# Kernel tuning notes

Hardware: AMD Instinct MI355X
Metric: run time of the kernel (lower is better)

## Reference

```python
import math
import jax, jax.numpy as jnp
import numpy as np

FACTOR = math.pi ** (-0.5)
C1 = math.sqrt(3.0 / 8.0) * FACTOR
C2 = math.sqrt(3.0 / 4.0) * FACTOR
EPS = 1e-9


def _cg_111():
    # Clebsch-Gordan <1 m1 ; 1 m2 | 1 m3>, indexed [m1+1, m2+1, m3+1]
    s = 1.0 / math.sqrt(2.0)
    cg = np.zeros((3, 3, 3), np.float32)
    cg[2, 1, 2] = s   # <1,1;1,0|1,1>
    cg[1, 2, 2] = -s  # <1,0;1,1|1,1>
    cg[2, 0, 1] = s   # <1,1;1,-1|1,0>
    cg[0, 2, 1] = -s  # <1,-1;1,1|1,0>
    cg[1, 0, 0] = s   # <1,0;1,-1|1,-1>
    cg[0, 1, 0] = -s  # <1,-1;1,0|1,-1>
    return jnp.asarray(cg)


def spherical_l1(r):
    # r: [n,p,q,3] -> Y1, Y2: [n,p,q,3] (real/imag parts of Y_1^m)
    rx, ry, rz = r[..., 0], r[..., 1], r[..., 2]
    Y1 = jnp.stack([C1 * rx, C2 * rz, -C1 * rx], axis=-1)
    Y2 = jnp.stack([-C1 * ry, jnp.zeros_like(ry), -C1 * ry], axis=-1)
    zero = (jnp.linalg.norm(r, axis=-1) == 0.0)[..., None]
    Y1 = jnp.where(zero, 1.0, Y1)
    Y2 = jnp.where(zero, 1.0, Y2)
    return Y1, Y2


def setup_inputs() -> dict:
    key = jax.random.key(0)
    ks = jax.random.split(key, 12)
    n, p, fr, fin, fout = 16, 256, 64, 64, 64
    rbf = jax.random.normal(ks[0], (n, p, p, fr), jnp.float32)
    uv = jax.random.normal(ks[1], (n, p, p, 3), jnp.float32)
    uv = uv / (jnp.linalg.norm(uv, axis=-1, keepdims=True) + 1e-12)
    inp1 = jax.random.normal(ks[2], (n, p, 3, fin), jnp.float32)
    inp2 = jax.random.normal(ks[3], (n, p, 3, fin), jnp.float32)
    mask = jnp.ones((n, p), jnp.bool_)
    sc = 0.08
    W1 = jax.random.normal(ks[4], (fin, fr), jnp.float32) * sc
    b1 = jax.random.normal(ks[5], (fin,), jnp.float32) * sc
    W2 = jax.random.normal(ks[6], (fin, fin), jnp.float32) * sc
    b2 = jax.random.normal(ks[7], (fin,), jnp.float32) * sc
    W_si = jax.random.normal(ks[8], (fout, fin), jnp.float32) * sc
    bias_b = jax.random.normal(ks[9], (1,), jnp.float32) * sc
    return {"rbf": rbf, "unit_vector": uv, "inp1": inp1, "inp2": inp2,
            "mask": mask, "coef": _cg_111(), "W1": W1, "b1": b1,
            "W2": W2, "b2": b2, "W_si": W_si, "bias_b": bias_b}


def reference(rbf, unit_vector, inp1, inp2, mask, coef, W1, b1, W2, b2, W_si, bias_b):
    m = mask[:, :, None, None]  # broadcast over q and last dims
    Y1, Y2 = spherical_l1(unit_vector)
    Y1 = jnp.where(m, Y1, 0.0)
    Y2 = jnp.where(m, Y2, 0.0)
    # radial embedding MLP: Linear -> ReLU -> Linear
    radial = jnp.einsum('npqr,fr->npqf', rbf, W1) + b1
    radial = jax.nn.relu(radial)
    radial = jnp.einsum('npqf,gf->npqg', radial, W2) + b2
    radial = jnp.where(m, radial, 0.0)

    def tp(Y, inp):
        return jnp.einsum('abc,npqb,npqf,npaf->nqcf', coef, Y, radial, inp,
                          optimize='optimal')

    out1 = tp(Y1, inp1) - tp(Y2, inp2)
    out2 = tp(Y2, inp1) + tp(Y1, inp2)
    # norm over {stack, c} dims, keepdim on c -> [n,q,1,f]
    norm = jnp.sqrt(jnp.sum(out1 ** 2 + out2 ** 2, axis=-2, keepdims=True))
    out1 = out1 / (norm + EPS)
    out2 = out2 / (norm + EPS)
    # gated self-interaction
    out1 = jnp.einsum('nqcf,gf->nqcg', out1, W_si)
    out2 = jnp.einsum('nqcf,gf->nqcg', out2, W_si)
    norm2 = jnp.sqrt(jnp.sum(out1 ** 2 + out2 ** 2, axis=-2))  # [n,q,g]
    nonlinear = jax.nn.relu(norm2 + bias_b[0])[:, :, None, :]  # [n,q,1,g]
    return out1 * nonlinear, out2 * nonlinear
```

## Files before the change

### kernel.cpp

```cpp
#include <hip/hip_runtime.h>
#include <hip/hip_bf16.h>

typedef __attribute__((ext_vector_type(8))) short short8;
typedef __attribute__((ext_vector_type(4))) float f32x4;
typedef __attribute__((ext_vector_type(4))) unsigned int u32x4;

#define MFMA16(A, B, C) __builtin_amdgcn_mfma_f32_16x16x32_bf16(A, B, C, 0, 0, 0)

__device__ __forceinline__ unsigned int pkbf(float lo, float hi) {
  unsigned int ul = (unsigned int)__bfloat16_as_ushort(__float2bfloat16(lo));
  unsigned int uh = (unsigned int)__bfloat16_as_ushort(__float2bfloat16(hi));
  return ul | (uh << 16);
}

union S8U { short8 s; u32x4 u; };
__device__ __forceinline__ short8 mk8(unsigned int a, unsigned int b,
                                      unsigned int c, unsigned int d) {
  S8U t; u32x4 v = {a, b, c, d}; t.u = v; return t.s;
}

constexpr float SU = 0.24430125595146f;
constexpr float SW = 0.34549414947134f;


__global__ __launch_bounds__(256) void tfield_partial(
    const float* __restrict__ rbf,  const float* __restrict__ uv,
    const float* __restrict__ inp1, const float* __restrict__ inp2,
    const float* __restrict__ W1,   const float* __restrict__ b1,
    const float* __restrict__ W2,   const float* __restrict__ b2,
    float* __restrict__ ws)
{
  __shared__ __align__(16) unsigned char pool[27008];
  unsigned int* wfrag = (unsigned int*)pool;
  unsigned int* hbuf  = (unsigned int*)(pool + 12288);
  float* ibuf  = (float*)(pool + 20480);
  float* biasL = (float*)(pool + 26624);
  float* accL  = (float*)pool;

  const int tid = threadIdx.x;
  const int l   = tid & 63;
  const int w   = tid >> 6;
  const int g   = l >> 4;
  const int qh  = l & 15;

  const int bid = blockIdx.x;
  const int wid = ((((bid & 7) << 5) | (bid >> 5)) << 2) | ((bid >> 3) & 3);
  const int nq  = wid >> 2;
  const int fh  = (wid >> 1) & 1;
  const int ph  = wid & 1;
  const int n   = nq >> 4;
  const int q0  = (nq & 15) << 4;

  #pragma unroll
  for (int k = 0; k < 3; ++k) {
    const int slot = tid + (k << 8);
    const int fi = slot >> 6;
    const int ll = slot & 63;
    const int gg = ll >> 4;
    const int qq = ll & 15;
    const float* src;
    if (fi < 8) {
      src = W1 + ((fi >> 1) * 16 + qq) * 64 + (fi & 1) * 32 + gg * 8;
    } else {
      const int fj = fi - 8;
      src = W2 + (((fh << 1) + (fj >> 1)) * 16 + qq) * 64 + (fj & 1) * 32 + gg * 8;
    }
    f32x4 x0 = *(const f32x4*)src;
    f32x4 x1 = *(const f32x4*)(src + 4);
    u32x4 vv = {pkbf(x0[0], x0[1]), pkbf(x0[2], x0[3]), pkbf(x1[0], x1[1]), pkbf(x1[2], x1[3])};
    *(u32x4*)(wfrag + ((fi << 6) + ll) * 4) = vv;
  }
  if (tid < 96) biasL[tid] = (tid < 64) ? b1[tid] : b2[(fh << 5) + tid - 64];
  __syncthreads();

  const float* bL1 = biasL;
  const float* bL2 = biasL + 64;

  f32x4 accT[2][6];
  #pragma unroll
  for (int a = 0; a < 2; ++a)
    #pragma unroll
    for (int j = 0; j < 6; ++j) accT[a][j] = (f32x4){0.f, 0.f, 0.f, 0.f};

  const size_t nbase = (size_t)n * 256;
  const int pbase = (ph << 7) + w;

  const int sl = (l < 24) ? l : l - 24;
  const float* isrcb = (l < 24) ? inp1 : inp2;
  const int ioff = (sl >> 3) * 64 + (fh << 5) + ((sl & 7) << 2);

  unsigned int* hrow = hbuf + (w << 9) + (qh << 5);
  float* iw = ibuf + w * 384;
  const int swz = qh & 7;

  f32x4 rn0, rn1, rn2, rn3;
  { const float* rr = rbf + ((nbase + pbase) * 256 + q0 + qh) * 64 + (g << 3);
    rn0 = *(const f32x4*)rr;        rn1 = *(const f32x4*)(rr + 4);
    rn2 = *(const f32x4*)(rr + 32); rn3 = *(const f32x4*)(rr + 36); }
  f32x4 stage_v = {0.f, 0.f, 0.f, 0.f};
  if (l < 48) stage_v = *(const f32x4*)(isrcb + (nbase + pbase) * 192 + ioff);
  float uc0, uc1, uc2, un0, un1, un2;
  { const float* u = uv + ((nbase + pbase) * 256 + q0 + qh) * 3;
    uc0 = u[0]; uc1 = u[1]; uc2 = u[2]; }

  short8 rf0 = mk8(pkbf(rn0[0], rn0[1]), pkbf(rn0[2], rn0[3]), pkbf(rn1[0], rn1[1]), pkbf(rn1[2], rn1[3]));
  short8 rf1 = mk8(pkbf(rn2[0], rn2[1]), pkbf(rn2[2], rn2[3]), pkbf(rn3[0], rn3[1]), pkbf(rn3[2], rn3[3]));
  f32x4 h4[4];
  #pragma unroll
  for (int mt = 0; mt < 4; ++mt) {
    f32x4 c = *(const f32x4*)(bL1 + (mt << 4) + (g << 2));
    short8 a0 = *(const short8*)(wfrag + (((mt << 1) + 0) * 64 + l) * 4);
    short8 a1 = *(const short8*)(wfrag + (((mt << 1) + 1) * 64 + l) * 4);
    c = MFMA16(a0, rf0, c);
    c = MFMA16(a1, rf1, c);
    h4[mt] = c;
  }
  if (l < 48) *(f32x4*)(iw + (l << 2)) = stage_v;
  #pragma unroll
  for (int mt = 0; mt < 4; ++mt) {
    const float e0 = fmaxf(h4[mt][0], 0.f);
    const float e1 = fmaxf(h4[mt][1], 0.f);
    const float e2 = fmaxf(h4[mt][2], 0.f);
    const float e3 = fmaxf(h4[mt][3], 0.f);
    const int base = ((((mt << 1) + (g >> 1)) ^ swz) << 2) + ((g & 1) << 1);
    hrow[base]     = pkbf(e0, e1);
    hrow[base + 1] = pkbf(e2, e3);
  }
  short8 hb0 = *(const short8*)(hrow + (((0 + g) ^ swz) << 2));
  short8 hb1 = *(const short8*)(hrow + (((4 + g) ^ swz) << 2));
  { const float* rr = rbf + ((nbase + pbase + 4) * 256 + q0 + qh) * 64 + (g << 3);
    rn0 = *(const f32x4*)rr;        rn1 = *(const f32x4*)(rr + 4);
    rn2 = *(const f32x4*)(rr + 32); rn3 = *(const f32x4*)(rr + 36); }
  if (l < 48) stage_v = *(const f32x4*)(isrcb + (nbase + pbase + 4) * 192 + ioff);
  { const float* u = uv + ((nbase + pbase + 4) * 256 + q0 + qh) * 3;
    un0 = u[0]; un1 = u[1]; un2 = u[2]; }

  for (int s = 0; s < 32; ++s) {
    const int s2 = (s + 2 < 32) ? s + 2 : 31;

    rf0 = mk8(pkbf(rn0[0], rn0[1]), pkbf(rn0[2], rn0[3]), pkbf(rn1[0], rn1[1]), pkbf(rn1[2], rn1[3]));
    rf1 = mk8(pkbf(rn2[0], rn2[1]), pkbf(rn2[2], rn2[3]), pkbf(rn3[0], rn3[1]), pkbf(rn3[2], rn3[3]));
    #pragma unroll
    for (int mt = 0; mt < 4; ++mt) {
      f32x4 c = *(const f32x4*)(bL1 + (mt << 4) + (g << 2));
      short8 a0 = *(const short8*)(wfrag + (((mt << 1) + 0) * 64 + l) * 4);
      short8 a1 = *(const short8*)(wfrag + (((mt << 1) + 1) * 64 + l) * 4);
      c = MFMA16(a0, rf0, c);
      c = MFMA16(a1, rf1, c);
      h4[mt] = c;
    }
    { const float* rr = rbf + ((nbase + pbase + (s2 << 2)) * 256 + q0 + qh) * 64 + (g << 3);
      rn0 = *(const f32x4*)rr;        rn1 = *(const f32x4*)(rr + 4);
      rn2 = *(const f32x4*)(rr + 32); rn3 = *(const f32x4*)(rr + 36); }

    f32x4 cc0, cc1;
    {
      f32x4 c = *(const f32x4*)(bL2 + (g << 2));
      short8 wa0 = *(const short8*)(wfrag + ((8 + 0) * 64 + l) * 4);
      short8 wa1 = *(const short8*)(wfrag + ((8 + 1) * 64 + l) * 4);
      c = MFMA16(wa0, hb0, c);
      c = MFMA16(wa1, hb1, c);
      cc0 = c;
      c = *(const f32x4*)(bL2 + 16 + (g << 2));
      wa0 = *(const short8*)(wfrag + ((8 + 2) * 64 + l) * 4);
      wa1 = *(const short8*)(wfrag + ((8 + 3) * 64 + l) * 4);
      c = MFMA16(wa0, hb0, c);
      c = MFMA16(wa1, hb1, c);
      cc1 = c;
    }

    const float su  = SU * uc0;
    const float sv  = SU * uc1;
    const float swc = SW * uc2;
    uc0 = un0; uc1 = un1; uc2 = un2;
    { const float* u = uv + ((nbase + pbase + (s2 << 2)) * 256 + q0 + qh) * 3;
      un0 = u[0]; un1 = u[1]; un2 = u[2]; }

    const float* ib = iw + ((s & 1) * 192) + (g << 2);
    #pragma unroll
    for (int mt2l = 0; mt2l < 2; ++mt2l) {
      const f32x4 A0 = *(const f32x4*)(ib + (mt2l << 4));
      const f32x4 A1 = *(const f32x4*)(ib + (mt2l << 4) + 32);
      const f32x4 A2 = *(const f32x4*)(ib + (mt2l << 4) + 64);
      const f32x4 B0 = *(const f32x4*)(ib + (mt2l << 4) + 96);
      const f32x4 B1 = *(const f32x4*)(ib + (mt2l << 4) + 128);
      const f32x4 B2 = *(const f32x4*)(ib + (mt2l << 4) + 160);
      const f32x4 cc = mt2l ? cc1 : cc0;

      const f32x4 t1 = su * A1, t2 = sv * B1;
      const f32x4 t3 = su * B1, t4 = sv * A1;
      const f32x4 g10 = (t1 + t2) - swc * A0;
      const f32x4 g11 = su * (A0 + A2) - sv * (B0 - B2);
      const f32x4 g12 = (t1 - t2) + swc * A2;
      const f32x4 g20 = (t3 - t4) - swc * B0;
      const f32x4 g21 = sv * (A0 - A2) + su * (B0 + B2);
      const f32x4 g22 = (t3 + t4) + swc * B2;
      accT[mt2l][0] += cc * g10;
      accT[mt2l][1] += cc * g11;
      accT[mt2l][2] += cc * g12;
      accT[mt2l][3] += cc * g20;
      accT[mt2l][4] += cc * g21;
      accT[mt2l][5] += cc * g22;
    }

    if (l < 48) *(f32x4*)(iw + (((s + 1) & 1) * 192) + (l << 2)) = stage_v;
    if (l < 48) stage_v = *(const f32x4*)(isrcb + (nbase + pbase + (s2 << 2)) * 192 + ioff);

    #pragma unroll
    for (int mt = 0; mt < 4; ++mt) {
      const float e0 = fmaxf(h4[mt][0], 0.f);
      const float e1 = fmaxf(h4[mt][1], 0.f);
      const float e2 = fmaxf(h4[mt][2], 0.f);
      const float e3 = fmaxf(h4[mt][3], 0.f);
      const int base = ((((mt << 1) + (g >> 1)) ^ swz) << 2) + ((g & 1) << 1);
      hrow[base]     = pkbf(e0, e1);
      hrow[base + 1] = pkbf(e2, e3);
    }
    hb0 = *(const short8*)(hrow + (((0 + g) ^ swz) << 2));
    hb1 = *(const short8*)(hrow + (((4 + g) ^ swz) << 2));
  }

  __syncthreads();
  for (int i = tid; i < 3072; i += 256) accL[i] = 0.f;
  __syncthreads();
  for (int t = 0; t < 4; ++t) {
    if (w == t) {
      #pragma unroll
      for (int mt2l = 0; mt2l < 2; ++mt2l)
        #pragma unroll
        for (int v = 0; v < 4; ++v) {
          float* dst = accL + (((qh << 5) + (mt2l << 4) + (g << 2) + v) * 6);
          #pragma unroll
          for (int j = 0; j < 6; ++j) dst[j] += accT[mt2l][j][v];
        }
    }
    __syncthreads();
  }
  float* wp = ws + (size_t)wid * 3072;
  for (int i = tid; i < 3072; i += 256) wp[i] = accL[i];
}

__global__ __launch_bounds__(512) void tfield_finish(
    const float* __restrict__ ws, const float* __restrict__ Wsi,
    const float* __restrict__ biasb, float* __restrict__ out)
{
  __shared__ __align__(16) float accL[6144];
  __shared__ __align__(16) float wsiT[4096];

  const int tid = threadIdx.x;
  const int l   = tid & 63;
  const int w   = tid >> 6;
  const int nq  = blockIdx.x;
  const int n   = nq >> 4;
  const int q0  = (nq & 15) << 4;

  const float* c00 = ws + (size_t)(nq * 4 + 0) * 3072;
  const float* c01 = c00 + 3072;
  const float* c10 = c00 + 6144;
  const float* c11 = c00 + 9216;
  for (int i = tid; i < 3072; i += 512) {
    const int qhh = i / 192;
    const int rem = i - qhh * 192;
    accL[qhh * 384 + rem]       = c00[i] + c01[i];
    accL[qhh * 384 + 192 + rem] = c10[i] + c11[i];
  }
  #pragma unroll
  for (int k = 0; k < 8; ++k) {
    const int f = (w << 3) + k;
    wsiT[(f << 6) + l] = Wsi[(l << 6) + f];
  }
  __syncthreads();

  #pragma unroll
  for (int rep = 0; rep < 2; ++rep) {
    const int qq = w + (rep << 3);
    float* xp = accL + ((qq << 6) + l) * 6;
    const float x0 = xp[0], x1 = xp[1], x2 = xp[2], x3 = xp[3], x4 = xp[4], x5 = xp[5];
    const float nrm = sqrtf(x0*x0 + x1*x1 + x2*x2 + x3*x3 + x4*x4 + x5*x5);
    const float sc = 1.f / (nrm + 1e-9f);
    xp[0] = x0 * sc; xp[1] = x1 * sc; xp[2] = x2 * sc;
    xp[3] = x3 * sc; xp[4] = x4 * sc; xp[5] = x5 * sc;
  }
  __syncthreads();

  const float bb = biasb[0];
  #pragma unroll
  for (int rep = 0; rep < 2; ++rep) {
    const int qq = w + (rep << 3);
    const float* arow = accL + (qq << 6) * 6;
    float pj0 = 0, pj1 = 0, pj2 = 0, pj3 = 0, pj4 = 0, pj5 = 0;
    for (int f = 0; f < 64; ++f) {
      const float wv = wsiT[(f << 6) + l];
      const float* ap = arow + f * 6;
      pj0 += ap[0] * wv; pj1 += ap[1] * wv; pj2 += ap[2] * wv;
      pj3 += ap[3] * wv; pj4 += ap[4] * wv; pj5 += ap[5] * wv;
    }
    const float s2 = pj0*pj0 + pj1*pj1 + pj2*pj2 + pj3*pj3 + pj4*pj4 + pj5*pj5;
    const float nl = fmaxf(sqrtf(s2) + bb, 0.f);
    const int q = q0 + qq;
    float* o1 = out + (size_t)((n * 256 + q) * 3) * 64 + l;
    float* o2 = o1 + 786432;
    o1[0]   = pj0 * nl;
    o1[64]  = pj1 * nl;
    o1[128] = pj2 * nl;
    o2[0]   = pj3 * nl;
    o2[64]  = pj4 * nl;
    o2[128] = pj5 * nl;
  }
}

__global__ __launch_bounds__(512) void tfield_kernel(
    const float* __restrict__ rbf,  const float* __restrict__ uv,
    const float* __restrict__ inp1, const float* __restrict__ inp2,
    const float* __restrict__ W1,   const float* __restrict__ b1,
    const float* __restrict__ W2,   const float* __restrict__ b2,
    const float* __restrict__ Wsi,  const float* __restrict__ biasb,
    float* __restrict__ out)
{
  __shared__ __align__(16) unsigned char pool[40960];
  unsigned int* wfrag = (unsigned int*)pool;
  unsigned int* hbuf  = (unsigned int*)(pool + 16384);
  float* accL = (float*)pool;
  float* wsiT = (float*)(pool + 24576);

  const int tid = threadIdx.x;
  const int l   = tid & 63;
  const int w   = tid >> 6;
  const int g   = l >> 4;
  const int qh  = l & 15;
  const int n   = blockIdx.x >> 4;
  const int q0  = (blockIdx.x & 15) << 4;

  {
    const int row = ((w >> 1) << 4) + qh;
    const int kb  = ((w & 1) << 5) + (g << 3);
    const float* s1 = W1 + row * 64 + kb;
    f32x4 x0 = *(const f32x4*)s1;
    f32x4 x1 = *(const f32x4*)(s1 + 4);
    u32x4 v1 = {pkbf(x0[0], x0[1]), pkbf(x0[2], x0[3]), pkbf(x1[0], x1[1]), pkbf(x1[2], x1[3])};
    *(u32x4*)(wfrag + ((w << 6) + l) * 4) = v1;
    const float* s2 = W2 + row * 64 + kb;
    x0 = *(const f32x4*)s2;
    x1 = *(const f32x4*)(s2 + 4);
    u32x4 v2 = {pkbf(x0[0], x0[1]), pkbf(x0[2], x0[3]), pkbf(x1[0], x1[1]), pkbf(x1[2], x1[3])};
    *(u32x4*)(wfrag + (((8 + w) << 6) + l) * 4) = v2;
  }
  __syncthreads();

  float accT[4][4][6];
  #pragma unroll
  for (int a = 0; a < 4; ++a)
    #pragma unroll
    for (int b = 0; b < 4; ++b)
      #pragma unroll
      for (int j = 0; j < 6; ++j) accT[a][b][j] = 0.f;

  const size_t nbase = (size_t)n * 256;
  const float* rr0 = rbf + ((nbase + w) * 256 + q0 + qh) * 64 + (g << 3);
  f32x4 nx0 = *(const f32x4*)(rr0);
  f32x4 nx1 = *(const f32x4*)(rr0 + 4);
  f32x4 nx2 = *(const f32x4*)(rr0 + 32);
  f32x4 nx3 = *(const f32x4*)(rr0 + 36);

  unsigned int* hrow = hbuf + ((w << 4) + qh) * 32;
  const int swz = qh & 7;

  for (int s = 0; s < 32; ++s) {
    const int p = (s << 3) + w;
    f32x4 r0 = nx0, r1 = nx1, r2 = nx2, r3 = nx3;
    {
      const int pn = (s < 31) ? p + 8 : p;
      const float* rr = rbf + ((nbase + pn) * 256 + q0 + qh) * 64 + (g << 3);
      nx0 = *(const f32x4*)(rr);
      nx1 = *(const f32x4*)(rr + 4);
      nx2 = *(const f32x4*)(rr + 32);
      nx3 = *(const f32x4*)(rr + 36);
    }
    const float* uvp = uv + ((nbase + p) * 256 + q0 + qh) * 3;
    const float su = SU * uvp[0];
    const float sv = SU * uvp[1];
    const float swc = SW * uvp[2];

    const short8 rf0 = mk8(pkbf(r0[0], r0[1]), pkbf(r0[2], r0[3]), pkbf(r1[0], r1[1]), pkbf(r1[2], r1[3]));
    const short8 rf1 = mk8(pkbf(r2[0], r2[1]), pkbf(r2[2], r2[3]), pkbf(r3[0], r3[1]), pkbf(r3[2], r3[3]));

    f32x4 h4[4];
    #pragma unroll
    for (int mt = 0; mt < 4; ++mt) {
      f32x4 c = *(const f32x4*)(b1 + (mt << 4) + (g << 2));
      short8 a0 = *(const short8*)(wfrag + (((mt << 1) + 0) * 64 + l) * 4);
      short8 a1 = *(const short8*)(wfrag + (((mt << 1) + 1) * 64 + l) * 4);
      c = MFMA16(a0, rf0, c);
      c = MFMA16(a1, rf1, c);
      h4[mt] = c;
    }
    #pragma unroll
    for (int mt = 0; mt < 4; ++mt) {
      const float e0 = fmaxf(h4[mt][0], 0.f);
      const float e1 = fmaxf(h4[mt][1], 0.f);
      const float e2 = fmaxf(h4[mt][2], 0.f);
      const float e3 = fmaxf(h4[mt][3], 0.f);
      const int base = ((((mt << 1) + (g >> 1)) ^ swz) << 2) + ((g & 1) << 1);
      hrow[base]     = pkbf(e0, e1);
      hrow[base + 1] = pkbf(e2, e3);
    }
    const short8 hb0 = *(const short8*)(hrow + (((0 + g) ^ swz) << 2));
    const short8 hb1 = *(const short8*)(hrow + (((4 + g) ^ swz) << 2));

    const float* i1p = inp1 + (nbase + p) * 192 + (g << 2);
    const float* i2p = inp2 + (nbase + p) * 192 + (g << 2);

    #pragma unroll
    for (int mt2 = 0; mt2 < 4; ++mt2) {
      f32x4 c = *(const f32x4*)(b2 + (mt2 << 4) + (g << 2));
      short8 wa0 = *(const short8*)(wfrag + ((8 + (mt2 << 1) + 0) * 64 + l) * 4);
      short8 wa1 = *(const short8*)(wfrag + ((8 + (mt2 << 1) + 1) * 64 + l) * 4);
      c = MFMA16(wa0, hb0, c);
      c = MFMA16(wa1, hb1, c);

      const int fo = mt2 << 4;
      const f32x4 A0 = *(const f32x4*)(i1p + fo);
      const f32x4 A1 = *(const f32x4*)(i1p + fo + 64);
      const f32x4 A2 = *(const f32x4*)(i1p + fo + 128);
      const f32x4 B0 = *(const f32x4*)(i2p + fo);
      const f32x4 B1 = *(const f32x4*)(i2p + fo + 64);
      const f32x4 B2 = *(const f32x4*)(i2p + fo + 128);
      const f32x4 a02p = A0 + A2, a02m = A0 - A2;
      const f32x4 b02p = B0 + B2, b02m = B0 - B2;

      #pragma unroll
      for (int v = 0; v < 4; ++v) {
        const float R = c[v];
        const float pua1 = su * A1[v], pvb1 = sv * B1[v];
        const float pub1 = su * B1[v], pva1 = sv * A1[v];
        const float g10 = pua1 - swc * A0[v] + pvb1;
        const float g11 = su * a02p[v] - sv * b02m[v];
        const float g12 = swc * A2[v] + pua1 - pvb1;
        const float g20 = pub1 - swc * B0[v] - pva1;
        const float g21 = sv * a02m[v] + su * b02p[v];
        const float g22 = swc * B2[v] + pub1 + pva1;
        accT[mt2][v][0] += R * g10;
        accT[mt2][v][1] += R * g11;
        accT[mt2][v][2] += R * g12;
        accT[mt2][v][3] += R * g20;
        accT[mt2][v][4] += R * g21;
        accT[mt2][v][5] += R * g22;
      }
    }
  }

  __syncthreads();
  for (int i = tid; i < 16 * 64 * 6; i += 512) accL[i] = 0.f;
  #pragma unroll
  for (int k = 0; k < 8; ++k) {
    const int f = (w << 3) + k;
    wsiT[(f << 6) + l] = Wsi[(l << 6) + f];
  }
  __syncthreads();

  for (int t = 0; t < 8; ++t) {
    if (w == t) {
      #pragma unroll
      for (int mt2 = 0; mt2 < 4; ++mt2)
        #pragma unroll
        for (int v = 0; v < 4; ++v) {
          float* dst = accL + (((qh << 6) + (mt2 << 4) + (g << 2) + v) * 6);
          #pragma unroll
          for (int j = 0; j < 6; ++j) dst[j] += accT[mt2][v][j];
        }
    }
    __syncthreads();
  }

  #pragma unroll
  for (int rep = 0; rep < 2; ++rep) {
    const int qq = w + (rep << 3);
    float* xp = accL + ((qq << 6) + l) * 6;
    const float x0 = xp[0], x1 = xp[1], x2 = xp[2], x3 = xp[3], x4 = xp[4], x5 = xp[5];
    const float nrm = sqrtf(x0*x0 + x1*x1 + x2*x2 + x3*x3 + x4*x4 + x5*x5);
    const float sc = 1.f / (nrm + 1e-9f);
    xp[0] = x0 * sc; xp[1] = x1 * sc; xp[2] = x2 * sc;
    xp[3] = x3 * sc; xp[4] = x4 * sc; xp[5] = x5 * sc;
  }
  __syncthreads();

  const float bb = biasb[0];
  #pragma unroll
  for (int rep = 0; rep < 2; ++rep) {
    const int qq = w + (rep << 3);
    const float* arow = accL + (qq << 6) * 6;
    float pj0 = 0, pj1 = 0, pj2 = 0, pj3 = 0, pj4 = 0, pj5 = 0;
    for (int f = 0; f < 64; ++f) {
      const float wv = wsiT[(f << 6) + l];
      const float* ap = arow + f * 6;
      pj0 += ap[0] * wv; pj1 += ap[1] * wv; pj2 += ap[2] * wv;
      pj3 += ap[3] * wv; pj4 += ap[4] * wv; pj5 += ap[5] * wv;
    }
    const float s2 = pj0*pj0 + pj1*pj1 + pj2*pj2 + pj3*pj3 + pj4*pj4 + pj5*pj5;
    const float nl = fmaxf(sqrtf(s2) + bb, 0.f);
    const int q = q0 + qq;
    float* o1 = out + (size_t)((n * 256 + q) * 3) * 64 + l;
    float* o2 = o1 + 786432;
    o1[0]   = pj0 * nl;
    o1[64]  = pj1 * nl;
    o1[128] = pj2 * nl;
    o2[0]   = pj3 * nl;
    o2[64]  = pj4 * nl;
    o2[128] = pj5 * nl;
  }
}

extern "C" void kernel_launch(void* const* d_in, const int* in_sizes, int n_in,
                              void* d_out, int out_size, void* d_ws, size_t ws_size,
                              hipStream_t stream) {
  (void)in_sizes; (void)n_in; (void)out_size;
  const size_t ws_needed = (size_t)1024 * 3072 * sizeof(float);
  if (ws_size >= ws_needed) {
    tfield_partial<<<dim3(1024), dim3(256), 0, stream>>>(
        (const float*)d_in[0], (const float*)d_in[1],
        (const float*)d_in[2], (const float*)d_in[3],
        (const float*)d_in[6], (const float*)d_in[7],
        (const float*)d_in[8], (const float*)d_in[9],
        (float*)d_ws);
    tfield_finish<<<dim3(256), dim3(512), 0, stream>>>(
        (const float*)d_ws, (const float*)d_in[10],
        (const float*)d_in[11], (float*)d_out);
  } else {
    tfield_kernel<<<dim3(256), dim3(512), 0, stream>>>(
        (const float*)d_in[0], (const float*)d_in[1],
        (const float*)d_in[2], (const float*)d_in[3],
        (const float*)d_in[6], (const float*)d_in[7],
        (const float*)d_in[8], (const float*)d_in[9],
        (const float*)d_in[10], (const float*)d_in[11],
        (float*)d_out);
  }
}
```

Measured before the change: 124.5 us.

## Merge output-feature halves into one block to avoid recomputing the radial MLP

```diff
diff --git a/kernel.cpp b/kernel.cpp
--- a/kernel.cpp
+++ b/kernel.cpp
@@ -30,11 +30,11 @@
     const float* __restrict__ W2,   const float* __restrict__ b2,
     float* __restrict__ ws)
 {
-  __shared__ __align__(16) unsigned char pool[27008];
+  __shared__ __align__(16) unsigned char pool[37376];
   unsigned int* wfrag = (unsigned int*)pool;
-  unsigned int* hbuf  = (unsigned int*)(pool + 12288);
-  float* ibuf  = (float*)(pool + 20480);
-  float* biasL = (float*)(pool + 26624);
+  unsigned int* hbuf  = (unsigned int*)(pool + 16384);
+  float* ibuf  = (float*)(pool + 24576);
+  float* biasL = (float*)(pool + 36864);
   float* accL  = (float*)pool;
 
   const int tid = threadIdx.x;
@@ -44,15 +44,14 @@
   const int qh  = l & 15;
 
   const int bid = blockIdx.x;
-  const int wid = ((((bid & 7) << 5) | (bid >> 5)) << 2) | ((bid >> 3) & 3);
-  const int nq  = wid >> 2;
-  const int fh  = (wid >> 1) & 1;
+  const int wid = ((bid & 7) << 6) | (bid >> 3);
+  const int nq  = wid >> 1;
   const int ph  = wid & 1;
   const int n   = nq >> 4;
   const int q0  = (nq & 15) << 4;
 
   #pragma unroll
-  for (int k = 0; k < 3; ++k) {
+  for (int k = 0; k < 4; ++k) {
     const int slot = tid + (k << 8);
     const int fi = slot >> 6;
     const int ll = slot & 63;
@@ -63,22 +62,22 @@
       src = W1 + ((fi >> 1) * 16 + qq) * 64 + (fi & 1) * 32 + gg * 8;
     } else {
       const int fj = fi - 8;
-      src = W2 + (((fh << 1) + (fj >> 1)) * 16 + qq) * 64 + (fj & 1) * 32 + gg * 8;
+      src = W2 + ((fj >> 1) * 16 + qq) * 64 + (fj & 1) * 32 + gg * 8;
     }
     f32x4 x0 = *(const f32x4*)src;
     f32x4 x1 = *(const f32x4*)(src + 4);
     u32x4 vv = {pkbf(x0[0], x0[1]), pkbf(x0[2], x0[3]), pkbf(x1[0], x1[1]), pkbf(x1[2], x1[3])};
     *(u32x4*)(wfrag + ((fi << 6) + ll) * 4) = vv;
   }
-  if (tid < 96) biasL[tid] = (tid < 64) ? b1[tid] : b2[(fh << 5) + tid - 64];
+  if (tid < 128) biasL[tid] = (tid < 64) ? b1[tid] : b2[tid - 64];
   __syncthreads();
 
   const float* bL1 = biasL;
   const float* bL2 = biasL + 64;
 
-  f32x4 accT[2][6];
-  #pragma unroll
-  for (int a = 0; a < 2; ++a)
+  f32x4 accT[4][6];
+  #pragma unroll
+  for (int a = 0; a < 4; ++a)
     #pragma unroll
     for (int j = 0; j < 6; ++j) accT[a][j] = (f32x4){0.f, 0.f, 0.f, 0.f};
 
@@ -87,18 +86,23 @@
 
   const int sl = (l < 24) ? l : l - 24;
   const float* isrcb = (l < 24) ? inp1 : inp2;
-  const int ioff = (sl >> 3) * 64 + (fh << 5) + ((sl & 7) << 2);
+  const int coff = (sl >> 3) * 64 + ((sl & 7) << 2);
+  const int ldst = (l < 24 ? 0 : 192) + coff;
 
   unsigned int* hrow = hbuf + (w << 9) + (qh << 5);
-  float* iw = ibuf + w * 384;
+  float* iw = ibuf + w * 768;
   const int swz = qh & 7;
 
   f32x4 rn0, rn1, rn2, rn3;
   { const float* rr = rbf + ((nbase + pbase) * 256 + q0 + qh) * 64 + (g << 3);
     rn0 = *(const f32x4*)rr;        rn1 = *(const f32x4*)(rr + 4);
     rn2 = *(const f32x4*)(rr + 32); rn3 = *(const f32x4*)(rr + 36); }
-  f32x4 stage_v = {0.f, 0.f, 0.f, 0.f};
-  if (l < 48) stage_v = *(const f32x4*)(isrcb + (nbase + pbase) * 192 + ioff);
+  f32x4 stage_v0 = {0.f,0.f,0.f,0.f}, stage_v1 = {0.f,0.f,0.f,0.f};
+  if (l < 48) {
+    const float* ip = isrcb + (nbase + pbase) * 192 + coff;
+    stage_v0 = *(const f32x4*)ip;
+    stage_v1 = *(const f32x4*)(ip + 32);
+  }
   float uc0, uc1, uc2, un0, un1, un2;
   { const float* u = uv + ((nbase + pbase) * 256 + q0 + qh) * 3;
     uc0 = u[0]; uc1 = u[1]; uc2 = u[2]; }
@@ -115,7 +119,10 @@
     c = MFMA16(a1, rf1, c);
     h4[mt] = c;
   }
-  if (l < 48) *(f32x4*)(iw + (l << 2)) = stage_v;
+  if (l < 48) {
+    *(f32x4*)(iw + ldst) = stage_v0;
+    *(f32x4*)(iw + ldst + 32) = stage_v1;
+  }
   #pragma unroll
   for (int mt = 0; mt < 4; ++mt) {
     const float e0 = fmaxf(h4[mt][0], 0.f);
@@ -131,7 +138,11 @@
   { const float* rr = rbf + ((nbase + pbase + 4) * 256 + q0 + qh) * 64 + (g << 3);
     rn0 = *(const f32x4*)rr;        rn1 = *(const f32x4*)(rr + 4);
     rn2 = *(const f32x4*)(rr + 32); rn3 = *(const f32x4*)(rr + 36); }
-  if (l < 48) stage_v = *(const f32x4*)(isrcb + (nbase + pbase + 4) * 192 + ioff);
+  if (l < 48) {
+    const float* ip = isrcb + (nbase + pbase + 4) * 192 + coff;
+    stage_v0 = *(const f32x4*)ip;
+    stage_v1 = *(const f32x4*)(ip + 32);
+  }
   { const float* u = uv + ((nbase + pbase + 4) * 256 + q0 + qh) * 3;
     un0 = u[0]; un1 = u[1]; un2 = u[2]; }
 
@@ -153,22 +164,6 @@
       rn0 = *(const f32x4*)rr;        rn1 = *(const f32x4*)(rr + 4);
       rn2 = *(const f32x4*)(rr + 32); rn3 = *(const f32x4*)(rr + 36); }
 
-    f32x4 cc0, cc1;
-    {
-      f32x4 c = *(const f32x4*)(bL2 + (g << 2));
-      short8 wa0 = *(const short8*)(wfrag + ((8 + 0) * 64 + l) * 4);
-      short8 wa1 = *(const short8*)(wfrag + ((8 + 1) * 64 + l) * 4);
-      c = MFMA16(wa0, hb0, c);
-      c = MFMA16(wa1, hb1, c);
-      cc0 = c;
-      c = *(const f32x4*)(bL2 + 16 + (g << 2));
-      wa0 = *(const short8*)(wfrag + ((8 + 2) * 64 + l) * 4);
-      wa1 = *(const short8*)(wfrag + ((8 + 3) * 64 + l) * 4);
-      c = MFMA16(wa0, hb0, c);
-      c = MFMA16(wa1, hb1, c);
-      cc1 = c;
-    }
-
     const float su  = SU * uc0;
     const float sv  = SU * uc1;
     const float swc = SW * uc2;
@@ -176,16 +171,22 @@
     { const float* u = uv + ((nbase + pbase + (s2 << 2)) * 256 + q0 + qh) * 3;
       un0 = u[0]; un1 = u[1]; un2 = u[2]; }
 
-    const float* ib = iw + ((s & 1) * 192) + (g << 2);
-    #pragma unroll
-    for (int mt2l = 0; mt2l < 2; ++mt2l) {
-      const f32x4 A0 = *(const f32x4*)(ib + (mt2l << 4));
-      const f32x4 A1 = *(const f32x4*)(ib + (mt2l << 4) + 32);
-      const f32x4 A2 = *(const f32x4*)(ib + (mt2l << 4) + 64);
-      const f32x4 B0 = *(const f32x4*)(ib + (mt2l << 4) + 96);
-      const f32x4 B1 = *(const f32x4*)(ib + (mt2l << 4) + 128);
-      const f32x4 B2 = *(const f32x4*)(ib + (mt2l << 4) + 160);
-      const f32x4 cc = mt2l ? cc1 : cc0;
+    const float* ib = iw + ((s & 1) * 384);
+    #pragma unroll
+    for (int mt2 = 0; mt2 < 4; ++mt2) {
+      f32x4 c = *(const f32x4*)(bL2 + (mt2 << 4) + (g << 2));
+      short8 wa0 = *(const short8*)(wfrag + ((8 + (mt2 << 1) + 0) * 64 + l) * 4);
+      short8 wa1 = *(const short8*)(wfrag + ((8 + (mt2 << 1) + 1) * 64 + l) * 4);
+      c = MFMA16(wa0, hb0, c);
+      c = MFMA16(wa1, hb1, c);
+
+      const int fo = (mt2 << 4) + (g << 2);
+      const f32x4 A0 = *(const f32x4*)(ib + fo);
+      const f32x4 A1 = *(const f32x4*)(ib + fo + 64);
+      const f32x4 A2 = *(const f32x4*)(ib + fo + 128);
+      const f32x4 B0 = *(const f32x4*)(ib + fo + 192);
+      const f32x4 B1 = *(const f32x4*)(ib + fo + 256);
+      const f32x4 B2 = *(const f32x4*)(ib + fo + 320);
 
       const f32x4 t1 = su * A1, t2 = sv * B1;
       const f32x4 t3 = su * B1, t4 = sv * A1;
@@ -195,16 +196,22 @@
       const f32x4 g20 = (t3 - t4) - swc * B0;
       const f32x4 g21 = sv * (A0 - A2) + su * (B0 + B2);
       const f32x4 g22 = (t3 + t4) + swc * B2;
-      accT[mt2l][0] += cc * g10;
-      accT[mt2l][1] += cc * g11;
-      accT[mt2l][2] += cc * g12;
-      accT[mt2l][3] += cc * g20;
-      accT[mt2l][4] += cc * g21;
-      accT[mt2l][5] += cc * g22;
-    }
-
-    if (l < 48) *(f32x4*)(iw + (((s + 1) & 1) * 192) + (l << 2)) = stage_v;
-    if (l < 48) stage_v = *(const f32x4*)(isrcb + (nbase + pbase + (s2 << 2)) * 192 + ioff);
+      accT[mt2][0] += c * g10;
+      accT[mt2][1] += c * g11;
+      accT[mt2][2] += c * g12;
+      accT[mt2][3] += c * g20;
+      accT[mt2][4] += c * g21;
+      accT[mt2][5] += c * g22;
+    }
+
+    if (l < 48) {
+      float* dst = iw + (((s + 1) & 1) * 384) + ldst;
+      *(f32x4*)dst = stage_v0;
+      *(f32x4*)(dst + 32) = stage_v1;
+      const float* ip = isrcb + (nbase + pbase + (s2 << 2)) * 192 + coff;
+      stage_v0 = *(const f32x4*)ip;
+      stage_v1 = *(const f32x4*)(ip + 32);
+    }
 
     #pragma unroll
     for (int mt = 0; mt < 4; ++mt) {
@@ -221,23 +228,23 @@
   }
 
   __syncthreads();
-  for (int i = tid; i < 3072; i += 256) accL[i] = 0.f;
+  for (int i = tid; i < 6144; i += 256) accL[i] = 0.f;
   __syncthreads();
   for (int t = 0; t < 4; ++t) {
     if (w == t) {
       #pragma unroll
-      for (int mt2l = 0; mt2l < 2; ++mt2l)
+      for (int mt2 = 0; mt2 < 4; ++mt2)
         #pragma unroll
         for (int v = 0; v < 4; ++v) {
-          float* dst = accL + (((qh << 5) + (mt2l << 4) + (g << 2) + v) * 6);
+          float* dst = accL + (((qh << 6) + (mt2 << 4) + (g << 2) + v) * 6);
           #pragma unroll
-          for (int j = 0; j < 6; ++j) dst[j] += accT[mt2l][j][v];
+          for (int j = 0; j < 6; ++j) dst[j] += accT[mt2][j][v];
         }
     }
     __syncthreads();
   }
-  float* wp = ws + (size_t)wid * 3072;
-  for (int i = tid; i < 3072; i += 256) wp[i] = accL[i];
+  float* wp = ws + (size_t)wid * 6144;
+  for (int i = tid; i < 6144; i += 256) wp[i] = accL[i];
 }
 
 __global__ __launch_bounds__(512) void tfield_finish(
@@ -254,16 +261,9 @@
   const int n   = nq >> 4;
   const int q0  = (nq & 15) << 4;
 
-  const float* c00 = ws + (size_t)(nq * 4 + 0) * 3072;
-  const float* c01 = c00 + 3072;
-  const float* c10 = c00 + 6144;
-  const float* c11 = c00 + 9216;
-  for (int i = tid; i < 3072; i += 512) {
-    const int qhh = i / 192;
-    const int rem = i - qhh * 192;
-    accL[qhh * 384 + rem]       = c00[i] + c01[i];
-    accL[qhh * 384 + 192 + rem] = c10[i] + c11[i];
-  }
+  const float* c0 = ws + (size_t)(nq * 2) * 6144;
+  const float* c1 = c0 + 6144;
+  for (int i = tid; i < 6144; i += 512) accL[i] = c0[i] + c1[i];
   #pragma unroll
   for (int k = 0; k < 8; ++k) {
     const int f = (w << 3) + k;
@@ -514,9 +514,9 @@
                               void* d_out, int out_size, void* d_ws, size_t ws_size,
                               hipStream_t stream) {
   (void)in_sizes; (void)n_in; (void)out_size;
-  const size_t ws_needed = (size_t)1024 * 3072 * sizeof(float);
+  const size_t ws_needed = (size_t)512 * 6144 * sizeof(float);
   if (ws_size >= ws_needed) {
-    tfield_partial<<<dim3(1024), dim3(256), 0, stream>>>(
+    tfield_partial<<<dim3(512), dim3(256), 0, stream>>>(
         (const float*)d_in[0], (const float*)d_in[1],
         (const float*)d_in[2], (const float*)d_in[3],
         (const float*)d_in[6], (const float*)d_in[7],
```

Result: faster. 117.3 us, median of 2 (-5.8%).
